# Optimization experiments

Measured on AMD Instinct MI355X. Metric: run time of the kernel, lower is better.

## Reference

```python
import jax, jax.numpy as jnp
import numpy as np

S = 7
NUM_CLASSES = 20
BATCH = 16384


def _iou(a, b):
    # a, b: [..., 4] boxes in (cx, cy, w, h) format
    ax1, ay1 = a[..., 0] - a[..., 2] / 2, a[..., 1] - a[..., 3] / 2
    ax2, ay2 = a[..., 0] + a[..., 2] / 2, a[..., 1] + a[..., 3] / 2
    bx1, by1 = b[..., 0] - b[..., 2] / 2, b[..., 1] - b[..., 3] / 2
    bx2, by2 = b[..., 0] + b[..., 2] / 2, b[..., 1] + b[..., 3] / 2
    iw = jnp.clip(jnp.minimum(ax2, bx2) - jnp.maximum(ax1, bx1), 0.0)
    ih = jnp.clip(jnp.minimum(ay2, by2) - jnp.maximum(ay1, by1), 0.0)
    inter = iw * ih
    union = a[..., 2] * a[..., 3] + b[..., 2] * b[..., 3] - inter
    return inter / (union + 1e-10)


def setup_inputs() -> dict:
    key = jax.random.key(0)
    k1, k2, k3, k4 = jax.random.split(key, 4)
    preds = jax.random.uniform(k1, (BATCH, S, S, 30), jnp.float32, 0.05, 0.95)
    box = jax.random.uniform(k2, (BATCH, S, S, 4), jnp.float32, 0.05, 0.95)
    conf = jax.random.bernoulli(k3, 0.3, (BATCH, S, S, 1)).astype(jnp.float32)
    cls = jax.random.uniform(k4, (BATCH, S, S, NUM_CLASSES), jnp.float32)
    labels = jnp.concatenate([box, conf, box, conf, cls], axis=-1)
    return {"preds": preds, "labels": labels}


def reference(preds, labels):
    obj = labels[..., 4] == 1.0          # [N, S, S] responsible-cell mask
    obj_f = obj.astype(preds.dtype)
    noobj_f = 1.0 - obj_f

    iou1 = _iou(preds[..., 0:4], labels[..., 0:4])
    iou2 = _iou(preds[..., 5:9], labels[..., 0:4])
    b1 = iou1 > iou2                      # box 1 is responsible
    b1f = b1.astype(preds.dtype)[..., None]

    # responsible / other box slices selected per cell
    p_xy = b1f * preds[..., 0:2] + (1 - b1f) * preds[..., 5:7]
    l_xy = b1f * labels[..., 0:2] + (1 - b1f) * labels[..., 5:7]
    p_wh = b1f * preds[..., 2:4] + (1 - b1f) * preds[..., 7:9]
    l_wh = b1f * labels[..., 2:4] + (1 - b1f) * labels[..., 7:9]
    conf_resp = jnp.where(b1, preds[..., 4], preds[..., 9])
    conf_other = jnp.where(b1, preds[..., 9], preds[..., 4])
    iou_resp = jnp.where(b1, iou1, iou2)
    iou_other = jnp.where(b1, iou2, iou1)

    loss_xy = 5.0 * jnp.sum(obj_f * jnp.sum((p_xy - l_xy) ** 2, axis=-1))
    loss_wh = jnp.sum(obj_f * jnp.sum((jnp.sqrt(p_wh) - jnp.sqrt(l_wh)) ** 2, axis=-1))
    loss_obj = jnp.sum(obj_f * (conf_resp - iou_resp) ** 2)
    loss_noobj_in = 0.5 * jnp.sum(obj_f * (conf_other - iou_other) ** 2)
    loss_noobj_out = 0.5 * jnp.sum(noobj_f * (preds[..., 4] ** 2 + preds[..., 9] ** 2))
    loss_cls = jnp.sum(obj_f * jnp.sum((preds[..., 10:] - labels[..., 10:]) ** 2, axis=-1))

    total = loss_xy + loss_wh + loss_obj + loss_noobj_in + loss_noobj_out + loss_cls
    return total / preds.shape[0]
```

## Files before the change

kernel.cpp:

```cpp
#include <hip/hip_runtime.h>

#define S 7
#define NUM_CLASSES 20
#define BATCH 16384
#define NCELLS (BATCH * S * S)
#define CPB 64
#define NTILES (NCELLS / CPB)
#define BLOCK 64
#define GRID 2560
#define TILE_FLOATS (CPB * 30)

typedef float f32x4 __attribute__((ext_vector_type(4)));
typedef float f32x2 __attribute__((ext_vector_type(2)));

__device__ __forceinline__ float iou_f(float acx, float acy, float aw, float ah,
                                       float bcx, float bcy, float bw, float bh) {
    float ax1 = acx - aw * 0.5f, ay1 = acy - ah * 0.5f;
    float ax2 = acx + aw * 0.5f, ay2 = acy + ah * 0.5f;
    float bx1 = bcx - bw * 0.5f, by1 = bcy - bh * 0.5f;
    float bx2 = bcx + bw * 0.5f, by2 = bcy + bh * 0.5f;
    float iw = fminf(ax2, bx2) - fmaxf(ax1, bx1);
    iw = fmaxf(iw, 0.0f);
    float ih = fminf(ay2, by2) - fmaxf(ay1, by1);
    ih = fmaxf(ih, 0.0f);
    float inter = iw * ih;
    float uni = aw * ah + bw * bh - inter;
    return inter / (uni + 1e-10f);
}

__device__ __forceinline__ float cell_loss(const float* cp, const float* cl) {
    float p[30], l[30];
    const float2* pp = (const float2*)cp;
    const float2* ll = (const float2*)cl;
#pragma unroll
    for (int j = 0; j < 15; ++j) {
        float2 v = pp[j];
        p[2 * j] = v.x; p[2 * j + 1] = v.y;
        float2 w = ll[j];
        l[2 * j] = w.x; l[2 * j + 1] = w.y;
    }

    float obj = (l[4] == 1.0f) ? 1.0f : 0.0f;

    float iou1 = iou_f(p[0], p[1], p[2], p[3], l[0], l[1], l[2], l[3]);
    float iou2 = iou_f(p[5], p[6], p[7], p[8], l[0], l[1], l[2], l[3]);
    bool b1 = iou1 > iou2;

    float pxy0 = b1 ? p[0] : p[5];
    float pxy1 = b1 ? p[1] : p[6];
    float pwh0 = b1 ? p[2] : p[7];
    float pwh1 = b1 ? p[3] : p[8];
    float conf_resp  = b1 ? p[4] : p[9];
    float conf_other = b1 ? p[9] : p[4];
    float iou_resp   = b1 ? iou1 : iou2;
    float iou_other  = b1 ? iou2 : iou1;

    float dx = pxy0 - l[0];
    float dy = pxy1 - l[1];
    float loss_xy = dx * dx + dy * dy;

    float sw0 = sqrtf(pwh0) - sqrtf(l[2]);
    float sw1 = sqrtf(pwh1) - sqrtf(l[3]);
    float loss_wh = sw0 * sw0 + sw1 * sw1;

    float d_obj = conf_resp - iou_resp;
    float loss_obj = d_obj * d_obj;

    float d_no = conf_other - iou_other;
    float loss_noobj_in = 0.5f * d_no * d_no;

    float loss_noobj_out = 0.5f * (1.0f - obj) * (p[4] * p[4] + p[9] * p[9]);

    float loss_cls = 0.0f;
#pragma unroll
    for (int c = 10; c < 30; ++c) {
        float d = p[c] - l[c];
        loss_cls += d * d;
    }

    return obj * (5.0f * loss_xy + loss_wh + loss_obj + loss_noobj_in + loss_cls)
         + loss_noobj_out;
}

__global__ __launch_bounds__(BLOCK, 2) void yolo_loss_kernel(
        const float* __restrict__ preds,
        const float* __restrict__ labels,
        float* __restrict__ out) {
    __shared__ __align__(16) float sp[TILE_FLOATS];
    __shared__ __align__(16) float sl[TILE_FLOATS];

    const int lane = threadIdx.x;
    float acc = 0.0f;

    for (int t = blockIdx.x; t < NTILES; t += GRID) {
        const float* gp = preds  + (size_t)t * TILE_FLOATS;
        const float* gl = labels + (size_t)t * TILE_FLOATS;

        f32x4 vp[7], vl[7];
#pragma unroll
        for (int j = 0; j < 7; ++j) {
            vp[j] = __builtin_nontemporal_load(&((const f32x4*)gp)[j * 64 + lane]);
            vl[j] = __builtin_nontemporal_load(&((const f32x4*)gl)[j * 64 + lane]);
        }
        f32x2 tp = __builtin_nontemporal_load(&((const f32x2*)(gp + 1792))[lane]);
        f32x2 tl = __builtin_nontemporal_load(&((const f32x2*)(gl + 1792))[lane]);

#pragma unroll
        for (int j = 0; j < 7; ++j) {
            ((f32x4*)sp)[j * 64 + lane] = vp[j];
            ((f32x4*)sl)[j * 64 + lane] = vl[j];
        }
        ((f32x2*)(sp + 1792))[lane] = tp;
        ((f32x2*)(sl + 1792))[lane] = tl;

        __syncthreads();

        acc += cell_loss(&sp[lane * 30], &sl[lane * 30]);

        __syncthreads();
    }

#pragma unroll
    for (int off = 32; off > 0; off >>= 1)
        acc += __shfl_down(acc, off, 64);
    if (lane == 0)
        atomicAdd(out, acc * (1.0f / (float)BATCH));
}

extern "C" void kernel_launch(void* const* d_in, const int* in_sizes, int n_in,
                              void* d_out, int out_size, void* d_ws, size_t ws_size,
                              hipStream_t stream) {
    const float* preds  = (const float*)d_in[0];
    const float* labels = (const float*)d_in[1];
    float* out = (float*)d_out;

    hipMemsetAsync(out, 0, sizeof(float), stream);

    yolo_loss_kernel<<<GRID, BLOCK, 0, stream>>>(preds, labels, out);
}
```

Baseline: 209.2 us.

## Prefetch next tile into registers while computing current tile, drop barriers

Restructures the grid-stride loop into a software pipeline. Each iteration issues the global loads for the next tile into registers, computes the loss on the tile already in LDS, then writes the prefetched data to LDS. It also removes both __syncthreads, relying on the block being a single 64-lane wavefront. The aim is to hide global memory latency, since the kernel has few waves per CU. In exchange it keeps more registers live and depends on in-order LDS behaviour within one wave.

```diff
diff --git a/kernel.cpp b/kernel.cpp
--- a/kernel.cpp
+++ b/kernel.cpp
@@ -92,39 +92,56 @@
     const int lane = threadIdx.x;
     float acc = 0.0f;
 
-    for (int t = blockIdx.x; t < NTILES; t += GRID) {
-        const float* gp = preds  + (size_t)t * TILE_FLOATS;
-        const float* gl = labels + (size_t)t * TILE_FLOATS;
+    int t = blockIdx.x;
+    const int iters = (NTILES - (int)blockIdx.x + GRID - 1) / GRID;
 
-        f32x4 vp[7], vl[7];
-#pragma unroll
-        for (int j = 0; j < 7; ++j) {
-            vp[j] = __builtin_nontemporal_load(&((const f32x4*)gp)[j * 64 + lane]);
-            vl[j] = __builtin_nontemporal_load(&((const f32x4*)gl)[j * 64 + lane]);
-        }
-        f32x2 tp = __builtin_nontemporal_load(&((const f32x2*)(gp + 1792))[lane]);
-        f32x2 tl = __builtin_nontemporal_load(&((const f32x2*)(gl + 1792))[lane]);
+    f32x4 vp[7], vl[7];
+    f32x2 tp, tl;
 
-#pragma unroll
-        for (int j = 0; j < 7; ++j) {
-            ((f32x4*)sp)[j * 64 + lane] = vp[j];
-            ((f32x4*)sl)[j * 64 + lane] = vl[j];
-        }
-        ((f32x2*)(sp + 1792))[lane] = tp;
-        ((f32x2*)(sl + 1792))[lane] = tl;
+#define LOAD_TILE(T)                                                           \
+    {                                                                          \
+        const float* gp = preds  + (size_t)(T) * TILE_FLOATS;                  \
+        const float* gl = labels + (size_t)(T) * TILE_FLOATS;                  \
+        _Pragma("unroll")                                                      \
+        for (int j = 0; j < 7; ++j) {                                          \
+            vp[j] = __builtin_nontemporal_load(&((const f32x4*)gp)[j * 64 + lane]); \
+            vl[j] = __builtin_nontemporal_load(&((const f32x4*)gl)[j * 64 + lane]); \
+        }                                                                      \
+        tp = __builtin_nontemporal_load(&((const f32x2*)(gp + 1792))[lane]);   \
+        tl = __builtin_nontemporal_load(&((const f32x2*)(gl + 1792))[lane]);   \
+    }
 
-        __syncthreads();
+#define WRITE_TILE()                                                           \
+    {                                                                          \
+        _Pragma("unroll")                                                      \
+        for (int j = 0; j < 7; ++j) {                                          \
+            ((f32x4*)sp)[j * 64 + lane] = vp[j];                               \
+            ((f32x4*)sl)[j * 64 + lane] = vl[j];                               \
+        }                                                                      \
+        ((f32x2*)(sp + 1792))[lane] = tp;                                      \
+        ((f32x2*)(sl + 1792))[lane] = tl;                                      \
+    }
 
+    LOAD_TILE(t);
+    WRITE_TILE();
+
+    for (int i = 1; i < iters; ++i) {
+        t += GRID;
+        LOAD_TILE(t);
         acc += cell_loss(&sp[lane * 30], &sl[lane * 30]);
+        WRITE_TILE();
+    }
 
-        __syncthreads();
-    }
+    acc += cell_loss(&sp[lane * 30], &sl[lane * 30]);
 
 #pragma unroll
     for (int off = 32; off > 0; off >>= 1)
         acc += __shfl_down(acc, off, 64);
     if (lane == 0)
         atomicAdd(out, acc * (1.0f / (float)BATCH));
+
+#undef LOAD_TILE
+#undef WRITE_TILE
 }
 
 extern "C" void kernel_launch(void* const* d_in, const int* in_sizes, int n_in,
```

Result: no change. 208.7 us (-0.3%).
